# Kernel tuning notes

Hardware: AMD Instinct MI355X
Metric: run time of the kernel (lower is better)

The kernel has to match this reference:

```python
import jax, jax.numpy as jnp
import numpy as np

B, S, E = 1, 2048, 2048
H, G, HD = 16, 4, 128  # heads, kv groups, head_dim; out_dim = H*HD = 2048
OUT_DIM = H * HD


def _rope_tables(seq_len, head_dim, base=10000.0):
    # Standard RoPE tables, full head_dim width (matches apply_rope's cos[:seq_len, :] of shape [S, HD])
    inv_freq = 1.0 / (base ** (np.arange(0, head_dim, 2, dtype=np.float32) / head_dim))
    t = np.arange(seq_len, dtype=np.float32)
    ang = np.outer(t, inv_freq)                      # [S, HD/2]
    ang = np.concatenate([ang, ang], axis=-1)        # [S, HD]
    return jnp.asarray(np.cos(ang)), jnp.asarray(np.sin(ang))


def setup_inputs() -> dict:
    key = jax.random.key(0)
    ks = jax.random.split(key, 6)
    x = jax.random.normal(ks[0], (B, S, E), dtype=jnp.float32)
    # causal mask: True above the diagonal => masked out (torch.triu(..., diagonal=1))
    mask = jnp.triu(jnp.ones((S, S), dtype=bool), k=1)
    cos, sin = _rope_tables(S, HD)
    scale = 0.02
    Wq = jax.random.normal(ks[1], (E, H * HD), dtype=jnp.float32) * scale
    Wk = jax.random.normal(ks[2], (E, G * HD), dtype=jnp.float32) * scale
    Wv = jax.random.normal(ks[3], (E, G * HD), dtype=jnp.float32) * scale
    Wout = jax.random.normal(ks[4], (H * HD, OUT_DIM), dtype=jnp.float32) * scale
    return {"x": x, "mask": mask, "cos": cos, "sin": sin,
            "Wq": Wq, "Wk": Wk, "Wv": Wv, "Wout": Wout}


def _apply_rope(t, cos, sin):
    # t: [B, h, S, HD]; cos/sin: [S, HD]
    hd = t.shape[-1]
    x1, x2 = t[..., : hd // 2], t[..., hd // 2 :]
    rotated = jnp.concatenate((-x2, x1), axis=-1)
    return t * cos[None, None] + rotated * sin[None, None]


def reference(x, mask, cos, sin, Wq, Wk, Wv, Wout):
    b, s, _ = x.shape
    q = (x @ Wq).reshape(b, s, H, HD).transpose(0, 2, 1, 3)   # [B,H,S,HD]
    k = (x @ Wk).reshape(b, s, G, HD).transpose(0, 2, 1, 3)   # [B,G,S,HD]
    v = (x @ Wv).reshape(b, s, G, HD).transpose(0, 2, 1, 3)
    q = _apply_rope(q, cos, sin)
    k = _apply_rope(k, cos, sin)
    rep = H // G
    k = jnp.repeat(k, rep, axis=1)                            # [B,H,S,HD]
    v = jnp.repeat(v, rep, axis=1)
    scores = jnp.einsum("bhqd,bhkd->bhqk", q, k)              # [B,H,S,S]
    scores = jnp.where(mask[None, None], -jnp.inf, scores)
    p = jax.nn.softmax(scores / jnp.sqrt(jnp.float32(HD)), axis=-1)
    o = jnp.einsum("bhqk,bhkd->bhqd", p, v)                   # [B,H,S,HD]
    o = o.transpose(0, 2, 1, 3).reshape(b, s, OUT_DIM)
    return (o @ Wout, p)
```

## Files before the change

### kernel.cpp

```cpp
#include <hip/hip_runtime.h>
#include <stdint.h>

#define S 2048
#define E 2048
#define NH 16
#define NG 4
#define HD 128
#define BK 64

using short8 = __attribute__((ext_vector_type(8))) short;
using f32x4  = __attribute__((ext_vector_type(4))) float;

__device__ __forceinline__ unsigned short f2bf(float f){
    union { float f; unsigned int i; } v; v.f = f;
    unsigned int x = v.i;
    unsigned int r = x + 0x7FFFu + ((x >> 16) & 1u);
    return (unsigned short)(r >> 16);
}

__device__ __forceinline__ void async_cp16(const unsigned short* g, unsigned short* l){
    __builtin_amdgcn_global_load_lds((const __attribute__((address_space(1))) void*)g,
                                     (__attribute__((address_space(3))) void*)l,
                                     16, 0, 0);
}

__device__ __forceinline__ void stage_tile_async(const unsigned short* __restrict__ G,
                                                 int ld, int k0,
                                                 unsigned short* lds)
{
    int tid = threadIdx.x;
    #pragma unroll
    for (int c = 0; c < 4; c++) {
        int e  = (c * 256 + tid) * 8;
        int r  = e >> 6;
        int cl = (e >> 3) & 7;
        int sc = cl ^ (r & 7);
        async_cp16(G + (size_t)r * ld + k0 + sc * 8, lds + e);
    }
}

__device__ __forceinline__ void stage_128x128(const unsigned short* __restrict__ G,
                                              int ld, unsigned short* lds)
{
    int tid = threadIdx.x;
    #pragma unroll
    for (int c = 0; c < 8; c++) {
        int e  = (c * 256 + tid) * 8;
        int r  = e >> 7;
        int cl = (e >> 3) & 15;
        int sc = cl ^ (r & 15);
        async_cp16(G + (size_t)r * ld + sc * 8, lds + e);
    }
}

__device__ __forceinline__ void stage_64x128(const unsigned short* __restrict__ G,
                                             int ld, unsigned short* lds)
{
    int tid = threadIdx.x;
    #pragma unroll
    for (int c = 0; c < 4; c++) {
        int e  = (c * 256 + tid) * 8;
        int r  = e >> 7;
        int cl = (e >> 3) & 15;
        int sc = cl ^ (r & 15);
        async_cp16(G + (size_t)r * ld + sc * 8, lds + e);
    }
}

__device__ __forceinline__ void gemm_core_async(const unsigned short* __restrict__ A, int lda,
                                                const unsigned short* __restrict__ Bt, int ldb,
                                                int K, f32x4 acc[4][4],
                                                unsigned short* lA, unsigned short* lB)
{
    int tid = threadIdx.x;
    int wave = tid >> 6, lane = tid & 63;
    int mBase = (wave >> 1) * 64, nBase = (wave & 1) * 64;
    int rowA = lane & 15, qc = lane >> 4;
    int nt = K / BK;
    stage_tile_async(A,  lda, 0, lA);
    stage_tile_async(Bt, ldb, 0, lB);
    __syncthreads();
    int cur = 0;
    for (int t = 0; t < nt; ++t) {
        if (t + 1 < nt) {
            stage_tile_async(A,  lda, (t + 1) * BK, lA + (cur ^ 1) * (128 * BK));
            stage_tile_async(Bt, ldb, (t + 1) * BK, lB + (cur ^ 1) * (128 * BK));
        }
        const unsigned short* cA = lA + cur * (128 * BK);
        const unsigned short* cB = lB + cur * (128 * BK);
        #pragma unroll
        for (int s = 0; s < 2; s++) {
            short8 af[4], bfr[4];
            #pragma unroll
            for (int i = 0; i < 4; i++) {
                int r  = mBase + i * 16 + rowA;
                int ch = (s * 4 + qc) ^ (r & 7);
                af[i] = *(const short8*)&cA[r * BK + ch * 8];
            }
            #pragma unroll
            for (int j = 0; j < 4; j++) {
                int r  = nBase + j * 16 + rowA;
                int ch = (s * 4 + qc) ^ (r & 7);
                bfr[j] = *(const short8*)&cB[r * BK + ch * 8];
            }
            #pragma unroll
            for (int i = 0; i < 4; i++)
                #pragma unroll
                for (int j = 0; j < 4; j++)
                    acc[i][j] = __builtin_amdgcn_mfma_f32_16x16x32_bf16(af[i], bfr[j], acc[i][j], 0, 0, 0);
        }
        __syncthreads();
        cur ^= 1;
    }
}

template<bool BF16OUT>
__device__ __forceinline__ void epilogue(f32x4 acc[4][4], void* Cv, int ldc,
                                         int row0, int col0, float scale)
{
    int tid = threadIdx.x, wave = tid >> 6, lane = tid & 63;
    int mBase = (wave >> 1) * 64, nBase = (wave & 1) * 64;
    int col = lane & 15, quad = lane >> 4;
    #pragma unroll
    for (int i = 0; i < 4; i++)
        #pragma unroll
        for (int j = 0; j < 4; j++)
            #pragma unroll
            for (int r = 0; r < 4; r++) {
                int gr = row0 + mBase + i * 16 + quad * 4 + r;
                int gc = col0 + nBase + j * 16 + col;
                float v = acc[i][j][r] * scale;
                if (BF16OUT) ((unsigned short*)Cv)[(size_t)gr * ldc + gc] = f2bf(v);
                else         ((float*)Cv)[(size_t)gr * ldc + gc] = v;
            }
}

template<bool BF16OUT>
__global__ __launch_bounds__(256) void gemm_mfma_as(const unsigned short* __restrict__ A, int lda,
                                                    const unsigned short* __restrict__ Bt, int ldb,
                                                    void* __restrict__ C, int ldc, int K)
{
    __shared__ unsigned short lA[2 * 128 * BK];
    __shared__ unsigned short lB[2 * 128 * BK];
    int row0 = blockIdx.y * 128, col0 = blockIdx.x * 128;
    f32x4 acc[4][4] = {};
    gemm_core_async(A + (size_t)row0 * lda, lda, Bt + (size_t)col0 * ldb, ldb, K, acc, lA, lB);
    epilogue<BF16OUT>(acc, C, ldc, row0, col0, 1.0f);
}

__device__ __forceinline__ float rmax16(float v){
    v = fmaxf(v, __shfl_xor(v, 1)); v = fmaxf(v, __shfl_xor(v, 2));
    v = fmaxf(v, __shfl_xor(v, 4)); v = fmaxf(v, __shfl_xor(v, 8));
    return v;
}
__device__ __forceinline__ float rsum16(float v){
    v += __shfl_xor(v, 1); v += __shfl_xor(v, 2);
    v += __shfl_xor(v, 4); v += __shfl_xor(v, 8);
    return v;
}

__device__ __forceinline__ void qk_compute(const short8 qf[4], const unsigned short* lK,
                                           int rowA, int quad, f32x4 sacc[8])
{
    #pragma unroll
    for (int j = 0; j < 8; j++)
        #pragma unroll
        for (int r = 0; r < 4; r++) sacc[j][r] = 0.f;
    #pragma unroll
    for (int ks = 0; ks < 4; ks++) {
        int ch = (ks * 4 + quad) ^ rowA;
        #pragma unroll
        for (int j = 0; j < 8; j++) {
            short8 kf = *(const short8*)&lK[(j * 16 + rowA) * 128 + ch * 8];
            sacc[j] = __builtin_amdgcn_mfma_f32_16x16x32_bf16(qf[ks], kf, sacc[j], 0, 0, 0);
        }
    }
}

__global__ __launch_bounds__(256, 2) void attn_flash(const unsigned short* __restrict__ Q,
                                                     const unsigned short* __restrict__ Kb,
                                                     const unsigned short* __restrict__ Vt,
                                                     unsigned short* __restrict__ Obf,
                                                     float* __restrict__ Mrow,
                                                     float* __restrict__ Li)
{
    __shared__ unsigned short lK[128 * 128];
    __shared__ unsigned short lV[128 * 128];
    __shared__ unsigned short lP[64 * 128];
    int h = blockIdx.x, qt = (gridDim.y - 1) - blockIdx.y, g = h >> 2;
    int jtm = qt >> 1;
    int rbase = (qt & 1) * 64;
    int tid = threadIdx.x, wave = tid >> 6, lane = tid & 63;
    int rowA = lane & 15, quad = lane >> 4;

    stage_64x128(Q + (size_t)(qt * 64) * (NH * HD) + h * HD, NH * HD, lK);
    __syncthreads();
    short8 qf[4];
    #pragma unroll
    for (int ks = 0; ks < 4; ks++) {
        int r = wave * 16 + rowA;
        int ch = (ks * 4 + quad) ^ rowA;
        qf[ks] = *(const short8*)&lK[r * 128 + ch * 8];
    }

    f32x4 m_, l_;
    #pragma unroll
    for (int r = 0; r < 4; r++) { m_[r] = -1e30f; l_[r] = 0.f; }
    f32x4 oacc[8];
    #pragma unroll
    for (int j = 0; j < 8; j++)
        #pragma unroll
        for (int r = 0; r < 4; r++) oacc[j][r] = 0.f;

    for (int jt = 0; jt <= jtm; ++jt) {
        __syncthreads();
        stage_128x128(Kb + (size_t)(jt * 128) * (NG * HD) + g * HD, NG * HD, lK);
        stage_128x128(Vt + (size_t)(g * HD) * S + jt * 128, S, lV);
        __syncthreads();
        f32x4 sacc[8];
        qk_compute(qf, lK, rowA, quad, sacc);
        if (jt == jtm) {
            #pragma unroll
            for (int j = 0; j < 8; j++)
                #pragma unroll
                for (int r = 0; r < 4; r++) {
                    int row = rbase + wave * 16 + quad * 4 + r;
                    int col = j * 16 + rowA;
                    if (col > row) sacc[j][r] = -1e30f;
                }
        }
        #pragma unroll
        for (int r = 0; r < 4; r++) {
            float tm = sacc[0][r];
            #pragma unroll
            for (int j = 1; j < 8; j++) tm = fmaxf(tm, sacc[j][r]);
            tm = rmax16(tm);
            float mn = fmaxf(m_[r], tm);
            float sc = __expf(m_[r] - mn);
            float es = 0.f;
            #pragma unroll
            for (int j = 0; j < 8; j++) {
                float p = __expf(sacc[j][r] - mn);
                sacc[j][r] = p;
                es += p;
            }
            es = rsum16(es);
            l_[r] = l_[r] * sc + es;
            m_[r] = mn;
            #pragma unroll
            for (int j = 0; j < 8; j++) oacc[j][r] *= sc;
        }
        #pragma unroll
        for (int j = 0; j < 8; j++)
            #pragma unroll
            for (int r = 0; r < 4; r++) {
                int row = wave * 16 + quad * 4 + r;
                int col = j * 16 + rowA;
                int ch = col >> 3;
                lP[row * 128 + (((ch ^ (row & 15)) << 3) | (col & 7))] = f2bf(sacc[j][r]);
            }
        __syncthreads();
        #pragma unroll
        for (int ks = 0; ks < 4; ks++) {
            int ch = (ks * 4 + quad) ^ rowA;
            short8 pa = *(const short8*)&lP[(wave * 16 + rowA) * 128 + ch * 8];
            #pragma unroll
            for (int j = 0; j < 8; j++) {
                short8 vb = *(const short8*)&lV[(j * 16 + rowA) * 128 + ch * 8];
                oacc[j] = __builtin_amdgcn_mfma_f32_16x16x32_bf16(pa, vb, oacc[j], 0, 0, 0);
            }
        }
    }

    f32x4 linv;
    #pragma unroll
    for (int r = 0; r < 4; r++) linv[r] = 1.0f / l_[r];

    #pragma unroll
    for (int j = 0; j < 8; j++)
        #pragma unroll
        for (int r = 0; r < 4; r++) {
            int row = qt * 64 + wave * 16 + quad * 4 + r;
            int col = h * HD + j * 16 + rowA;
            Obf[(size_t)row * (NH * HD) + col] = f2bf(oacc[j][r] * linv[r]);
        }

    if (rowA == 0) {
        int grow0 = qt * 64 + wave * 16 + quad * 4;
        #pragma unroll
        for (int r = 0; r < 4; r++) {
            Mrow[(size_t)h * S + grow0 + r] = m_[r];
            Li[(size_t)h * S + grow0 + r]  = linv[r];
        }
    }
}

__global__ __launch_bounds__(256) void p_write(const unsigned short* __restrict__ Q,
                                               const unsigned short* __restrict__ Kb,
                                               const float* __restrict__ Mrow,
                                               const float* __restrict__ Li,
                                               float* __restrict__ P)
{
    int jt = blockIdx.x, it = blockIdx.y, h = blockIdx.z;
    float* Pt = P + (size_t)h * S * S + (size_t)(it * 128) * S + jt * 128;
    int tid = threadIdx.x;
    if (jt > it) {
        #pragma unroll
        for (int q = 0; q < 16; q++) {
            int e4 = q * 256 + tid;
            int r  = e4 >> 5;
            int c4 = (e4 & 31) * 4;
            *(float4*)(Pt + (size_t)r * S + c4) = make_float4(0.f, 0.f, 0.f, 0.f);
        }
        return;
    }
    __shared__ unsigned short lA[2 * 128 * BK];
    __shared__ unsigned short lB[2 * 128 * BK];
    f32x4 acc[4][4] = {};
    gemm_core_async(Q + (size_t)(it * 128) * (NH * HD) + h * HD, NH * HD,
                    Kb + (size_t)(jt * 128) * (NG * HD) + (h >> 2) * HD, NG * HD,
                    HD, acc, lA, lB);
    int wave = tid >> 6, lane = tid & 63;
    int mBase = (wave >> 1) * 64, nBase = (wave & 1) * 64;
    int col = lane & 15, quad = lane >> 4;
    bool diag = (jt == it);
    #pragma unroll
    for (int i = 0; i < 4; i++) {
        float mm[4], li[4];
        #pragma unroll
        for (int r = 0; r < 4; r++) {
            int gr = it * 128 + mBase + i * 16 + quad * 4 + r;
            mm[r] = Mrow[(size_t)h * S + gr];
            li[r] = Li[(size_t)h * S + gr];
        }
        #pragma unroll
        for (int j = 0; j < 4; j++)
            #pragma unroll
            for (int r = 0; r < 4; r++) {
                int lr = mBase + i * 16 + quad * 4 + r;
                int lc = nBase + j * 16 + col;
                float v = (diag && lc > lr) ? 0.f
                          : __expf(acc[i][j][r] - mm[r]) * li[r];
                Pt[(size_t)lr * S + lc] = v;
            }
    }
}

__global__ __launch_bounds__(256) void transpose_cvt(const float* __restrict__ in,
                                                     unsigned short* __restrict__ out,
                                                     int R, int C, int inLd)
{
    __shared__ float t[32][33];
    int r0 = blockIdx.y * 32, c0 = blockIdx.x * 32;
    int tid = threadIdx.x;
    int rr = tid >> 3, cc = (tid & 7) * 4;
    float4 v = *(const float4*)(in + (size_t)(r0 + rr) * inLd + c0 + cc);
    t[rr][cc] = v.x; t[rr][cc + 1] = v.y; t[rr][cc + 2] = v.z; t[rr][cc + 3] = v.w;
    __syncthreads();
    int oc = tid >> 3, orr = (tid & 7) * 4;
    ushort4 o;
    o.x = f2bf(t[orr][oc]);     o.y = f2bf(t[orr + 1][oc]);
    o.z = f2bf(t[orr + 2][oc]); o.w = f2bf(t[orr + 3][oc]);
    *(ushort4*)(out + (size_t)(c0 + oc) * R + r0 + orr) = o;
}

__global__ __launch_bounds__(256) void cvt_bf16(const float* __restrict__ in,
                                                unsigned short* __restrict__ out, int n)
{
    int i = (blockIdx.x * 256 + threadIdx.x) * 8;
    if (i >= n) return;
    float4 a = *(const float4*)(in + i);
    float4 b = *(const float4*)(in + i + 4);
    unsigned int w0 = (unsigned int)f2bf(a.x) | ((unsigned int)f2bf(a.y) << 16);
    unsigned int w1 = (unsigned int)f2bf(a.z) | ((unsigned int)f2bf(a.w) << 16);
    unsigned int w2 = (unsigned int)f2bf(b.x) | ((unsigned int)f2bf(b.y) << 16);
    unsigned int w3 = (unsigned int)f2bf(b.z) | ((unsigned int)f2bf(b.w) << 16);
    *(uint4*)(out + i) = make_uint4(w0, w1, w2, w3);
}

__global__ void rope_bf16(const float* __restrict__ T, unsigned short* __restrict__ Tb,
                          const float* __restrict__ cosp, const float* __restrict__ sinp,
                          int nHeads, int inLd, int inOff, int outLd, float scale, int total)
{
    int idx = blockIdx.x * blockDim.x + threadIdx.x;
    if (idx >= total) return;
    int d = idx & 63;
    int head = (idx >> 6) % nHeads;
    int s = idx / (nHeads * 64);
    float c  = cosp[s * HD + d];
    float sn = sinp[s * HD + d];
    const float* ib = T + (size_t)s * inLd + inOff + head * HD + d;
    float x1 = ib[0], x2 = ib[64];
    unsigned short* ob = Tb + (size_t)s * outLd + head * HD + d;
    ob[0]  = f2bf((x1 * c - x2 * sn) * scale);
    ob[64] = f2bf((x2 * c + x1 * sn) * scale);
}

extern "C" void kernel_launch(void* const* d_in, const int* in_sizes, int n_in,
                              void* d_out, int out_size, void* d_ws, size_t ws_size,
                              hipStream_t stream)
{
    const float* x    = (const float*)d_in[0];
    const float* cosp = (const float*)d_in[2];
    const float* sinp = (const float*)d_in[3];
    const float* Wq   = (const float*)d_in[4];
    const float* Wk   = (const float*)d_in[5];
    const float* Wv   = (const float*)d_in[6];
    const float* Wout = (const float*)d_in[7];

    float* out0 = (float*)d_out;
    float* Pout = out0 + (size_t)S * E;

    unsigned short* Wqkvt = (unsigned short*)d_ws;
    unsigned short* Qbf   = Wqkvt + (size_t)3072 * E;
    unsigned short* Kbf   = Qbf   + (size_t)S * E;
    unsigned short* Vt    = Kbf   + (size_t)S * (NG * HD);
    unsigned short* Obf   = Vt    + (size_t)(NG * HD) * S;
    float* QKVb = (float*)(Obf + (size_t)S * E);
    float* Mrow = QKVb + (size_t)S * 3072;
    float* Li   = Mrow + (size_t)NH * S;
    unsigned short* xbf   = Obf;
    unsigned short* Woutt = (unsigned short*)QKVb;

    dim3 blk(256);
    transpose_cvt<<<dim3(E / 32, E / 32), blk, 0, stream>>>(Wq, Wqkvt, E, E, E);
    transpose_cvt<<<dim3((NG * HD) / 32, E / 32), blk, 0, stream>>>(Wk, Wqkvt + (size_t)E * E, E, NG * HD, NG * HD);
    transpose_cvt<<<dim3((NG * HD) / 32, E / 32), blk, 0, stream>>>(Wv, Wqkvt + (size_t)(E + NG * HD) * E, E, NG * HD, NG * HD);
    cvt_bf16<<<dim3((S * E) / (256 * 8)), blk, 0, stream>>>(x, xbf, S * E);

    gemm_mfma_as<false><<<dim3(3072 / 128, S / 128), blk, 0, stream>>>(xbf, E, Wqkvt, E, QKVb, 3072, E);

    rope_bf16<<<(S * NH * 64 + 255) / 256, blk, 0, stream>>>(QKVb, Qbf, cosp, sinp, NH, 3072, 0, NH * HD,
                                                             0.08838834764831845f, S * NH * 64);
    rope_bf16<<<(S * NG * 64 + 255) / 256, blk, 0, stream>>>(QKVb, Kbf, cosp, sinp, NG, 3072, E, NG * HD,
                                                             1.0f, S * NG * 64);
    transpose_cvt<<<dim3((NG * HD) / 32, S / 32), blk, 0, stream>>>(QKVb + E + NG * HD, Vt, S, NG * HD, 3072);

    transpose_cvt<<<dim3(E / 32, E / 32), blk, 0, stream>>>(Wout, Woutt, E, E, E);

    attn_flash<<<dim3(NH, S / 64), blk, 0, stream>>>(Qbf, Kbf, Vt, Obf, Mrow, Li);

    p_write<<<dim3(S / 128, S / 128, NH), blk, 0, stream>>>(Qbf, Kbf, Mrow, Li, Pout);

    gemm_mfma_as<false><<<dim3(E / 128, S / 128), blk, 0, stream>>>(Obf, E, Woutt, E, out0, E, E);
}
```

Baseline: 490.5 us.

## Fuse RoPE and V transpose into QKV GEMM epilogue; add MFMA priority hints

The QKV projection GEMM now writes its tile to shared memory and applies RoPE plus scaling for Q/K, or transposes V, directly in the epilogue. This removes the fp32 QKV intermediate buffer and three separate launches for rope and transpose. The workspace is reorganised so xbf and Woutt no longer alias other buffers. It also raises wave priority around the MFMA loops in the attention kernel. The tile staging goes through 64KB of LDS, and cos/sin are read uncoalesced per element.

```diff
diff --git a/kernel.cpp b/kernel.cpp
--- a/kernel.cpp
+++ b/kernel.cpp
@@ -148,6 +148,84 @@
     epilogue<BF16OUT>(acc, C, ldc, row0, col0, 1.0f);
 }
 
+__global__ __launch_bounds__(256) void qkv_gemm_fused(const unsigned short* __restrict__ A,
+                                                      const unsigned short* __restrict__ Bt,
+                                                      const float* __restrict__ cosp,
+                                                      const float* __restrict__ sinp,
+                                                      unsigned short* __restrict__ Qbf,
+                                                      unsigned short* __restrict__ Kbf,
+                                                      unsigned short* __restrict__ Vt)
+{
+    __shared__ unsigned short smem[4 * 128 * BK];
+    unsigned short* lA = smem;
+    unsigned short* lB = smem + 2 * 128 * BK;
+    int row0 = blockIdx.y * 128, col0 = blockIdx.x * 128;
+    f32x4 acc[4][4] = {};
+    gemm_core_async(A + (size_t)row0 * E, E, Bt + (size_t)col0 * E, E, E, acc, lA, lB);
+
+    float* ct = (float*)smem;
+    int tid = threadIdx.x, wave = tid >> 6, lane = tid & 63;
+    int mBase = (wave >> 1) * 64, nBase = (wave & 1) * 64;
+    int colI = lane & 15, quad = lane >> 4;
+    #pragma unroll
+    for (int i = 0; i < 4; i++)
+        #pragma unroll
+        for (int j = 0; j < 4; j++)
+            #pragma unroll
+            for (int r = 0; r < 4; r++)
+                ct[(mBase + i * 16 + quad * 4 + r) * 128 + (nBase + j * 16 + colI)] = acc[i][j][r];
+    __syncthreads();
+
+    int sect = blockIdx.x;
+    if (sect < 20) {
+        bool isQ = (sect < 16);
+        unsigned short* out = isQ ? Qbf : Kbf;
+        int outLd = isQ ? (NH * HD) : (NG * HD);
+        int hoff  = isQ ? sect * HD : (sect - 16) * HD;
+        float SC  = isQ ? 0.08838834764831845f : 1.0f;
+        #pragma unroll
+        for (int k = 0; k < 8; k++) {
+            int chunk = k * 256 + tid;
+            int row = chunk >> 4;
+            int d0  = (chunk & 15) * 8;
+            int srow = row0 + row;
+            unsigned int w[4];
+            #pragma unroll
+            for (int e2 = 0; e2 < 4; e2++) {
+                unsigned short h2[2];
+                #pragma unroll
+                for (int u = 0; u < 2; u++) {
+                    int d = d0 + e2 * 2 + u;
+                    float xv = ct[row * 128 + d];
+                    float c  = cosp[(size_t)srow * HD + d];
+                    float sn = sinp[(size_t)srow * HD + d];
+                    float partner = (d < 64) ? -ct[row * 128 + d + 64]
+                                             :  ct[row * 128 + d - 64];
+                    h2[u] = f2bf((xv * c + partner * sn) * SC);
+                }
+                w[e2] = (unsigned int)h2[0] | ((unsigned int)h2[1] << 16);
+            }
+            *(uint4*)&out[(size_t)srow * outLd + hoff + d0] = make_uint4(w[0], w[1], w[2], w[3]);
+        }
+    } else {
+        int dg0 = (sect - 20) * 128;
+        int d   = tid >> 1;
+        int sc0 = (tid & 1) * 64;
+        #pragma unroll
+        for (int k = 0; k < 8; k++) {
+            int s0 = sc0 + k * 8;
+            unsigned int w[4];
+            #pragma unroll
+            for (int e2 = 0; e2 < 4; e2++) {
+                unsigned short a0 = f2bf(ct[(s0 + e2 * 2) * 128 + d]);
+                unsigned short a1 = f2bf(ct[(s0 + e2 * 2 + 1) * 128 + d]);
+                w[e2] = (unsigned int)a0 | ((unsigned int)a1 << 16);
+            }
+            *(uint4*)&Vt[(size_t)(dg0 + d) * S + row0 + s0] = make_uint4(w[0], w[1], w[2], w[3]);
+        }
+    }
+}
+
 __device__ __forceinline__ float rmax16(float v){
     v = fmaxf(v, __shfl_xor(v, 1)); v = fmaxf(v, __shfl_xor(v, 2));
     v = fmaxf(v, __shfl_xor(v, 4)); v = fmaxf(v, __shfl_xor(v, 8));
@@ -166,6 +244,7 @@
     for (int j = 0; j < 8; j++)
         #pragma unroll
         for (int r = 0; r < 4; r++) sacc[j][r] = 0.f;
+    __builtin_amdgcn_s_setprio(1);
     #pragma unroll
     for (int ks = 0; ks < 4; ks++) {
         int ch = (ks * 4 + quad) ^ rowA;
@@ -175,6 +254,7 @@
             sacc[j] = __builtin_amdgcn_mfma_f32_16x16x32_bf16(qf[ks], kf, sacc[j], 0, 0, 0);
         }
     }
+    __builtin_amdgcn_s_setprio(0);
 }
 
 __global__ __launch_bounds__(256, 2) void attn_flash(const unsigned short* __restrict__ Q,
@@ -260,6 +340,7 @@
                 lP[row * 128 + (((ch ^ (row & 15)) << 3) | (col & 7))] = f2bf(sacc[j][r]);
             }
         __syncthreads();
+        __builtin_amdgcn_s_setprio(1);
         #pragma unroll
         for (int ks = 0; ks < 4; ks++) {
             int ch = (ks * 4 + quad) ^ rowA;
@@ -270,6 +351,7 @@
                 oacc[j] = __builtin_amdgcn_mfma_f32_16x16x32_bf16(pa, vb, oacc[j], 0, 0, 0);
             }
         }
+        __builtin_amdgcn_s_setprio(0);
     }
 
     f32x4 linv;
@@ -378,24 +460,6 @@
     *(uint4*)(out + i) = make_uint4(w0, w1, w2, w3);
 }
 
-__global__ void rope_bf16(const float* __restrict__ T, unsigned short* __restrict__ Tb,
-                          const float* __restrict__ cosp, const float* __restrict__ sinp,
-                          int nHeads, int inLd, int inOff, int outLd, float scale, int total)
-{
-    int idx = blockIdx.x * blockDim.x + threadIdx.x;
-    if (idx >= total) return;
-    int d = idx & 63;
-    int head = (idx >> 6) % nHeads;
-    int s = idx / (nHeads * 64);
-    float c  = cosp[s * HD + d];
-    float sn = sinp[s * HD + d];
-    const float* ib = T + (size_t)s * inLd + inOff + head * HD + d;
-    float x1 = ib[0], x2 = ib[64];
-    unsigned short* ob = Tb + (size_t)s * outLd + head * HD + d;
-    ob[0]  = f2bf((x1 * c - x2 * sn) * scale);
-    ob[64] = f2bf((x2 * c + x1 * sn) * scale);
-}
-
 extern "C" void kernel_launch(void* const* d_in, const int* in_sizes, int n_in,
                               void* d_out, int out_size, void* d_ws, size_t ws_size,
                               hipStream_t stream)
@@ -412,31 +476,23 @@
     float* Pout = out0 + (size_t)S * E;
 
     unsigned short* Wqkvt = (unsigned short*)d_ws;
-    unsigned short* Qbf   = Wqkvt + (size_t)3072 * E;
+    unsigned short* Woutt = Wqkvt + (size_t)3072 * E;
+    unsigned short* xbf   = Woutt + (size_t)E * E;
+    unsigned short* Qbf   = xbf   + (size_t)S * E;
     unsigned short* Kbf   = Qbf   + (size_t)S * E;
     unsigned short* Vt    = Kbf   + (size_t)S * (NG * HD);
     unsigned short* Obf   = Vt    + (size_t)(NG * HD) * S;
-    float* QKVb = (float*)(Obf + (size_t)S * E);
-    float* Mrow = QKVb + (size_t)S * 3072;
+    float* Mrow = (float*)(Obf + (size_t)S * E);
     float* Li   = Mrow + (size_t)NH * S;
-    unsigned short* xbf   = Obf;
-    unsigned short* Woutt = (unsigned short*)QKVb;
 
     dim3 blk(256);
     transpose_cvt<<<dim3(E / 32, E / 32), blk, 0, stream>>>(Wq, Wqkvt, E, E, E);
     transpose_cvt<<<dim3((NG * HD) / 32, E / 32), blk, 0, stream>>>(Wk, Wqkvt + (size_t)E * E, E, NG * HD, NG * HD);
     transpose_cvt<<<dim3((NG * HD) / 32, E / 32), blk, 0, stream>>>(Wv, Wqkvt + (size_t)(E + NG * HD) * E, E, NG * HD, NG * HD);
+    transpose_cvt<<<dim3(E / 32, E / 32), blk, 0, stream>>>(Wout, Woutt, E, E, E);
     cvt_bf16<<<dim3((S * E) / (256 * 8)), blk, 0, stream>>>(x, xbf, S * E);
 
-    gemm_mfma_as<false><<<dim3(3072 / 128, S / 128), blk, 0, stream>>>(xbf, E, Wqkvt, E, QKVb, 3072, E);
-
-    rope_bf16<<<(S * NH * 64 + 255) / 256, blk, 0, stream>>>(QKVb, Qbf, cosp, sinp, NH, 3072, 0, NH * HD,
-                                                             0.08838834764831845f, S * NH * 64);
-    rope_bf16<<<(S * NG * 64 + 255) / 256, blk, 0, stream>>>(QKVb, Kbf, cosp, sinp, NG, 3072, E, NG * HD,
-                                                             1.0f, S * NG * 64);
-    transpose_cvt<<<dim3((NG * HD) / 32, S / 32), blk, 0, stream>>>(QKVb + E + NG * HD, Vt, S, NG * HD, 3072);
-
-    transpose_cvt<<<dim3(E / 32, E / 32), blk, 0, stream>>>(Wout, Woutt, E, E, E);
+    qkv_gemm_fused<<<dim3(3072 / 128, S / 128), blk, 0, stream>>>(xbf, Wqkvt, cosp, sinp, Qbf, Kbf, Vt);
 
     attn_flash<<<dim3(NH, S / 64), blk, 0, stream>>>(Qbf, Kbf, Vt, Obf, Mrow, Li);
 
```

After: 511.1 us. 4.2% more time.
